# Kernel tuning notes

Hardware: AMD Instinct MI355X
Metric: run time of the kernel (lower is better)

The kernel has to match this reference:

```python
import jax, jax.numpy as jnp
import numpy as np

TEMPERATURE = 0.07
EPS = 1e-12  # F.normalize eps


def setup_inputs() -> dict:
    key = jax.random.key(0)
    k1, k2 = jax.random.split(key)
    features = jax.random.normal(k1, (16, 512, 768), dtype=jnp.float32)
    labels = jax.random.randint(k2, (16, 512), 0, 10, dtype=jnp.int64)
    return {"features": features, "labels": labels}


def reference(features, labels):
    B, S, H = features.shape
    x = features.reshape(-1, H)                       # [N, H], N = B*S
    lab = labels.reshape(-1)                          # [N]
    # F.normalize(dim=-1): divide by clamped L2 norm
    norm = jnp.maximum(jnp.linalg.norm(x, axis=-1, keepdims=True), EPS)
    x = x / norm
    sim = jnp.matmul(x, x.T) / TEMPERATURE            # [N, N]
    label_mask = (lab[None, :] == lab[:, None]).astype(sim.dtype)  # [N, N]
    n_pos = jnp.sum(label_mask)
    n_neg = label_mask.size - n_pos
    # masked means (equivalent to sim[mask].mean() / sim[~mask].mean())
    pos_mean = jnp.sum(sim * label_mask) / n_pos
    neg_mean = (jnp.sum(sim) - jnp.sum(sim * label_mask)) / n_neg
    # -log(exp(p) / (exp(p) + exp(n))) == logaddexp(0, n - p)
    loss = jnp.logaddexp(jnp.zeros((), sim.dtype), neg_mean - pos_mean)
    return loss
```

## Files before the change

### kernel.cpp

```cpp
#include <hip/hip_runtime.h>
#include <math.h>


#define NCLS 10
#define HDIM 768
#define HV4  (HDIM / 4)
#define CLS_FLOATS (NCLS * HDIM)
#define PBLK 256
#define RPB  32
#define PSLICES 8
#define NCHUNK (CLS_FLOATS / 256)

__global__ __launch_bounds__(768) void k1_fused(
    const float* __restrict__ x, const int* __restrict__ lab,
    float* __restrict__ partials) {
  __shared__ float srn[RPB];
  __shared__ int   slab[RPB];
  const int tid = threadIdx.x, lane = tid & 63, wave = tid >> 6;
  const int row0 = blockIdx.x * RPB;
  const float4* __restrict__ x4 = (const float4*)x;

  for (int r = wave; r < RPB; r += 12) {
    const int row = row0 + r;
    const size_t b = (size_t)row * HV4;
    const float4 t0 = x4[b + lane];
    const float4 t1 = x4[b + 64 + lane];
    const float4 t2 = x4[b + 128 + lane];
    float ss = t0.x * t0.x + t0.y * t0.y + t0.z * t0.z + t0.w * t0.w +
               t1.x * t1.x + t1.y * t1.y + t1.z * t1.z + t1.w * t1.w +
               t2.x * t2.x + t2.y * t2.y + t2.z * t2.z + t2.w * t2.w;
#pragma unroll
    for (int off = 32; off >= 1; off >>= 1) ss += __shfl_xor(ss, off, 64);
    if (lane == 0) {
      srn[r] = 1.0f / fmaxf(sqrtf(ss), 1e-12f);
      slab[r] = lab[row];
    }
  }
  __syncthreads();

  float acc[NCLS];
#pragma unroll
  for (int c = 0; c < NCLS; ++c) acc[c] = 0.0f;

  for (int rb = 0; rb < RPB; rb += 8) {
    float v[8];
#pragma unroll
    for (int u = 0; u < 8; ++u)
      v[u] = x[(size_t)(row0 + rb + u) * HDIM + tid];
#pragma unroll
    for (int u = 0; u < 8; ++u) {
      const float s = srn[rb + u];
      const int c = __builtin_amdgcn_readfirstlane(slab[rb + u]);
      const float p = v[u] * s;
      switch (c) {
        case 0: acc[0] += p; break;
        case 1: acc[1] += p; break;
        case 2: acc[2] += p; break;
        case 3: acc[3] += p; break;
        case 4: acc[4] += p; break;
        case 5: acc[5] += p; break;
        case 6: acc[6] += p; break;
        case 7: acc[7] += p; break;
        case 8: acc[8] += p; break;
        default: acc[9] += p; break;
      }
    }
  }

  float* __restrict__ outp = partials + (size_t)blockIdx.x * CLS_FLOATS;
#pragma unroll
  for (int c = 0; c < NCLS; ++c) outp[c * HDIM + tid] = acc[c];
}

__global__ __launch_bounds__(256) void k2_reduce(
    const float* __restrict__ partials, float* __restrict__ csum8) {
  const int chunk = blockIdx.x % NCHUNK;
  const int slice = blockIdx.x / NCHUNK;
  const int idx = chunk * 256 + threadIdx.x;
  const int p0 = slice * (PBLK / PSLICES);
  float s[4] = {0.f, 0.f, 0.f, 0.f};
  for (int p = p0; p < p0 + PBLK / PSLICES; p += 4) {
#pragma unroll
    for (int u = 0; u < 4; ++u)
      s[u] += partials[(size_t)(p + u) * CLS_FLOATS + idx];
  }
  csum8[(size_t)slice * CLS_FLOATS + idx] = (s[0] + s[1]) + (s[2] + s[3]);
}

__global__ __launch_bounds__(512) void k3_final(
    const float* __restrict__ csum8, const int* __restrict__ lab,
    float* __restrict__ out, int N) {
  __shared__ int scnt[NCLS];
  __shared__ double r0s[8], r1s[8];
  const int tid = threadIdx.x, lane = tid & 63, wave = tid >> 6;
  if (tid < NCLS) scnt[tid] = 0;
  __syncthreads();

  int cnt[NCLS];
#pragma unroll
  for (int c = 0; c < NCLS; ++c) cnt[c] = 0;
  for (int i = tid; i < N; i += blockDim.x) {
    const int l = lab[i];
#pragma unroll
    for (int c = 0; c < NCLS; ++c) cnt[c] += (l == c);
  }
#pragma unroll
  for (int c = 0; c < NCLS; ++c) {
    int v = cnt[c];
#pragma unroll
    for (int off = 32; off >= 1; off >>= 1) v += __shfl_xor(v, off, 64);
    if (lane == 0) atomicAdd(&scnt[c], v);
  }

  double masked = 0.0, total = 0.0;
  for (int h = tid; h < HDIM; h += blockDim.x) {
    double tv = 0.0;
#pragma unroll
    for (int c = 0; c < NCLS; ++c) {
      double sv = 0.0;
#pragma unroll
      for (int sl = 0; sl < PSLICES; ++sl)
        sv += (double)csum8[(size_t)sl * CLS_FLOATS + c * HDIM + h];
      masked += sv * sv;
      tv += sv;
    }
    total += tv * tv;
  }
#pragma unroll
  for (int off = 32; off >= 1; off >>= 1) {
    masked += __shfl_xor(masked, off, 64);
    total  += __shfl_xor(total,  off, 64);
  }
  if (lane == 0) { r0s[wave] = masked; r1s[wave] = total; }
  __syncthreads();
  if (tid == 0) {
    double m = 0.0, t = 0.0;
    const int nw = blockDim.x >> 6;
    for (int w = 0; w < nw; ++w) { m += r0s[w]; t += r1s[w]; }
    double n_pos = 0.0;
    for (int c = 0; c < NCLS; ++c) { const double cc = scnt[c]; n_pos += cc * cc; }
    const double T = 0.07;
    const double nn = (double)N * (double)N;
    const double pos_mean = m / (T * n_pos);
    const double neg_mean = (t - m) / (T * (nn - n_pos));
    const double d = neg_mean - pos_mean;
    out[0] = (float)(fmax(d, 0.0) + log1p(exp(-fabs(d))));
  }
}

extern "C" void kernel_launch(void* const* d_in, const int* in_sizes, int n_in,
                              void* d_out, int out_size, void* d_ws, size_t ws_size,
                              hipStream_t stream) {
  const float* x = (const float*)d_in[0];
  const int* lab = (const int*)d_in[1];
  const int N = in_sizes[1];

  float* partials = (float*)d_ws;
  float* csum8 = partials + (size_t)PBLK * CLS_FLOATS;

  k1_fused<<<PBLK, HDIM, 0, stream>>>(x, lab, partials);
  k2_reduce<<<NCHUNK * PSLICES, 256, 0, stream>>>(partials, csum8);
  k3_final<<<1, 512, 0, stream>>>(csum8, lab, (float*)d_out, N);
}
```

Measured before the change: 89.30 us.

## Collapse partial reduction into full per-column-slice reduction with squared sums

Replaces the sliced partial-sum reduction and the heavy single-block final pass with a kernel where each of 24 blocks fully reduces all 256 partial rows for a 32-column slice. Each block then computes the masked and total squared sums in double precision. The final kernel only adds 24 pairs of doubles and counts the labels. This removes the single-block 768x10x8 read and the intermediate csum8 buffer. In exchange only 24 blocks are launched, so the bandwidth-heavy reduction may use the GPU's compute units poorly.

```diff
diff --git a/kernel.cpp b/kernel.cpp
--- a/kernel.cpp
+++ b/kernel.cpp
@@ -6,10 +6,12 @@
 #define HDIM 768
 #define HV4  (HDIM / 4)
 #define CLS_FLOATS (NCLS * HDIM)
+#define CLS_F4 (CLS_FLOATS / 4)
+#define HD_F4  (HDIM / 4)
 #define PBLK 256
 #define RPB  32
-#define PSLICES 8
-#define NCHUNK (CLS_FLOATS / 256)
+#define K2BLK 24
+#define K2THR 512
 
 __global__ __launch_bounds__(768) void k1_fused(
     const float* __restrict__ x, const int* __restrict__ lab,
@@ -72,27 +74,87 @@
   for (int c = 0; c < NCLS; ++c) outp[c * HDIM + tid] = acc[c];
 }
 
-__global__ __launch_bounds__(256) void k2_reduce(
-    const float* __restrict__ partials, float* __restrict__ csum8) {
-  const int chunk = blockIdx.x % NCHUNK;
-  const int slice = blockIdx.x / NCHUNK;
-  const int idx = chunk * 256 + threadIdx.x;
-  const int p0 = slice * (PBLK / PSLICES);
-  float s[4] = {0.f, 0.f, 0.f, 0.f};
-  for (int p = p0; p < p0 + PBLK / PSLICES; p += 4) {
-#pragma unroll
-    for (int u = 0; u < 4; ++u)
-      s[u] += partials[(size_t)(p + u) * CLS_FLOATS + idx];
-  }
-  csum8[(size_t)slice * CLS_FLOATS + idx] = (s[0] + s[1]) + (s[2] + s[3]);
+__global__ __launch_bounds__(K2THR) void k2_full(
+    const float* __restrict__ partials, double* __restrict__ bsums) {
+  const float4* __restrict__ p4 = (const float4*)partials;
+  const int tid = threadIdx.x, lane = tid & 63, wave = tid >> 6;
+  const int f  = tid & 7;
+  const int pg = tid >> 3;
+  const int h04 = blockIdx.x * 8;
+
+  float4 acc[NCLS];
+#pragma unroll
+  for (int c = 0; c < NCLS; ++c) acc[c] = make_float4(0.f, 0.f, 0.f, 0.f);
+
+  const size_t base = (size_t)(pg * 4) * CLS_F4 + (size_t)h04 + f;
+#pragma unroll
+  for (int pp = 0; pp < 4; ++pp) {
+#pragma unroll
+    for (int c = 0; c < NCLS; ++c) {
+      const float4 v = p4[base + (size_t)pp * CLS_F4 + c * HD_F4];
+      acc[c].x += v.x; acc[c].y += v.y; acc[c].z += v.z; acc[c].w += v.w;
+    }
+  }
+
+#pragma unroll
+  for (int c = 0; c < NCLS; ++c) {
+#pragma unroll
+    for (int off = 8; off <= 32; off <<= 1) {
+      acc[c].x += __shfl_xor(acc[c].x, off, 64);
+      acc[c].y += __shfl_xor(acc[c].y, off, 64);
+      acc[c].z += __shfl_xor(acc[c].z, off, 64);
+      acc[c].w += __shfl_xor(acc[c].w, off, 64);
+    }
+  }
+
+  __shared__ float4 sred[K2THR / 64][NCLS][8];
+  if (lane < 8) {
+#pragma unroll
+    for (int c = 0; c < NCLS; ++c) sred[wave][c][lane] = acc[c];
+  }
+  __syncthreads();
+
+  __shared__ float4 sS[NCLS][8];
+  if (tid < NCLS * 8) {
+    const int c = tid >> 3, ff = tid & 7;
+    float4 s = sred[0][c][ff];
+#pragma unroll
+    for (int w = 1; w < K2THR / 64; ++w) {
+      const float4 v = sred[w][c][ff];
+      s.x += v.x; s.y += v.y; s.z += v.z; s.w += v.w;
+    }
+    sS[c][ff] = s;
+  }
+  __syncthreads();
+
+  __shared__ double smm[8], stt[8];
+  if (tid < 8) {
+    double m = 0.0, t0 = 0.0, t1 = 0.0, t2 = 0.0, t3 = 0.0;
+#pragma unroll
+    for (int c = 0; c < NCLS; ++c) {
+      const float4 s = sS[c][tid];
+      m += (double)s.x * s.x + (double)s.y * s.y +
+           (double)s.z * s.z + (double)s.w * s.w;
+      t0 += s.x; t1 += s.y; t2 += s.z; t3 += s.w;
+    }
+    smm[tid] = m;
+    stt[tid] = t0 * t0 + t1 * t1 + t2 * t2 + t3 * t3;
+  }
+  __syncthreads();
+  if (tid == 0) {
+    double m = 0.0, t = 0.0;
+#pragma unroll
+    for (int i = 0; i < 8; ++i) { m += smm[i]; t += stt[i]; }
+    bsums[(size_t)blockIdx.x * 2]     = m;
+    bsums[(size_t)blockIdx.x * 2 + 1] = t;
+  }
 }
 
 __global__ __launch_bounds__(512) void k3_final(
-    const float* __restrict__ csum8, const int* __restrict__ lab,
+    const double* __restrict__ bsums, const int* __restrict__ lab,
     float* __restrict__ out, int N) {
   __shared__ int scnt[NCLS];
-  __shared__ double r0s[8], r1s[8];
-  const int tid = threadIdx.x, lane = tid & 63, wave = tid >> 6;
+  const int tid = threadIdx.x, lane = tid & 63;
   if (tid < NCLS) scnt[tid] = 0;
   __syncthreads();
 
@@ -111,32 +173,15 @@
     for (int off = 32; off >= 1; off >>= 1) v += __shfl_xor(v, off, 64);
     if (lane == 0) atomicAdd(&scnt[c], v);
   }
-
-  double masked = 0.0, total = 0.0;
-  for (int h = tid; h < HDIM; h += blockDim.x) {
-    double tv = 0.0;
-#pragma unroll
-    for (int c = 0; c < NCLS; ++c) {
-      double sv = 0.0;
-#pragma unroll
-      for (int sl = 0; sl < PSLICES; ++sl)
-        sv += (double)csum8[(size_t)sl * CLS_FLOATS + c * HDIM + h];
-      masked += sv * sv;
-      tv += sv;
-    }
-    total += tv * tv;
-  }
-#pragma unroll
-  for (int off = 32; off >= 1; off >>= 1) {
-    masked += __shfl_xor(masked, off, 64);
-    total  += __shfl_xor(total,  off, 64);
-  }
-  if (lane == 0) { r0s[wave] = masked; r1s[wave] = total; }
-  __syncthreads();
+  __syncthreads();
+
   if (tid == 0) {
     double m = 0.0, t = 0.0;
-    const int nw = blockDim.x >> 6;
-    for (int w = 0; w < nw; ++w) { m += r0s[w]; t += r1s[w]; }
+#pragma unroll
+    for (int b = 0; b < K2BLK; ++b) {
+      m += bsums[2 * b];
+      t += bsums[2 * b + 1];
+    }
     double n_pos = 0.0;
     for (int c = 0; c < NCLS; ++c) { const double cc = scnt[c]; n_pos += cc * cc; }
     const double T = 0.07;
@@ -156,9 +201,9 @@
   const int N = in_sizes[1];
 
   float* partials = (float*)d_ws;
-  float* csum8 = partials + (size_t)PBLK * CLS_FLOATS;
+  double* bsums = (double*)(partials + (size_t)PBLK * CLS_FLOATS);
 
   k1_fused<<<PBLK, HDIM, 0, stream>>>(x, lab, partials);
-  k2_reduce<<<NCHUNK * PSLICES, 256, 0, stream>>>(partials, csum8);
-  k3_final<<<1, 512, 0, stream>>>(csum8, lab, (float*)d_out, N);
-}
+  k2_full<<<K2BLK, K2THR, 0, stream>>>(partials, bsums);
+  k3_final<<<1, 512, 0, stream>>>(bsums, lab, (float*)d_out, N);
+}
```

Result: no change. 89.25 us, median of 2 (-0.1%).
